# Optimization experiments

Hardware: AMD Instinct MI355X
Metric: run time of the kernel (lower is better)

Reference implementation:

```python
import jax, jax.numpy as jnp
import numpy as np


def setup_inputs() -> dict:
    key = jax.random.key(0)
    k1, k2, k3, k4, k5 = jax.random.split(key, 5)
    B, T, K, H, A = 16, 256, 256, 512, 49
    return {
        "hiddens_des": jax.random.normal(k1, (B, K, H), dtype=jnp.float32),
        "hiddens_title": jax.random.normal(k2, (B, T, H), dtype=jnp.float32),
        "Wv": jax.random.normal(k3, (A, H), dtype=jnp.float32) * (1.0 / np.sqrt(H)),
        "Wg": jax.random.normal(k4, (A, H), dtype=jnp.float32) * (1.0 / np.sqrt(H)),
        "Wh": jax.random.normal(k5, (1, A), dtype=jnp.float32) * (1.0 / np.sqrt(A)),
    }


def reference(hiddens_des, hiddens_title, Wv, Wg, Wh):
    # Dropout is identity (eval mode) for the deterministic baseline.
    # content_v: (B,1,K,49) + (B,T,1,49) -> (B,T,K,49)
    cv = jnp.einsum("bkh,ah->bka", hiddens_des, Wv)    # (B,K,49)
    cg = jnp.einsum("bth,ah->bta", hiddens_title, Wg)  # (B,T,49)
    content = cv[:, None, :, :] + cg[:, :, None, :]     # (B,T,K,49)
    z = jnp.einsum("btka,a->btk", jnp.tanh(content), Wh[0])  # (B,T,K)
    alpha = jax.nn.softmax(z, axis=-1)                  # softmax over K
    c_hat = jnp.einsum("btk,bkh->bth", alpha, hiddens_des)  # (B,T,H)
    return (c_hat, alpha)
```

## Files before the change

### kernel.cpp

```cpp
#include <hip/hip_runtime.h>
#include <hip/hip_bf16.h>

#define B_ 16
#define T_ 256
#define K_ 256
#define H_ 512
#define A_ 49
#define APAD 64

typedef __attribute__((ext_vector_type(8))) short short8;
typedef __attribute__((ext_vector_type(4))) float f32x4;

__device__ __forceinline__ ushort f2bf(float f) {
    uint u = __builtin_bit_cast(uint, f);
    u += 0x7FFF + ((u >> 16) & 1);
    return (ushort)(u >> 16);
}

__device__ __forceinline__ void cvt_hilo(float4 v0, float4 v1, short8& hi, short8& lo) {
    float v[8] = {v0.x, v0.y, v0.z, v0.w, v1.x, v1.y, v1.z, v1.w};
    #pragma unroll
    for (int i = 0; i < 8; ++i) {
        ushort h = f2bf(v[i]);
        float hf = __builtin_bit_cast(float, (uint)h << 16);
        hi[i] = (short)h;
        lo[i] = (short)f2bf(v[i] - hf);
    }
}

__device__ __forceinline__ float sig2(float x) {
    float e = __expf(2.f * x);
    return __builtin_amdgcn_rcpf(e + 1.f);
}

__global__ __launch_bounds__(256) void kW(const float* __restrict__ Wv,
                                          const float* __restrict__ Wg,
                                          ushort* __restrict__ Whl)
{
    int blk = blockIdx.x;
    int m = blk >> 6, row = blk & 63;
    const float* W = m ? Wg : Wv;
    int tid = threadIdx.x;
    ushort* hi = Whl + ((size_t)(m * 2 + 0) * 64 + row) * H_;
    ushort* lo = Whl + ((size_t)(m * 2 + 1) * 64 + row) * H_;
    #pragma unroll
    for (int c = tid; c < H_; c += 256) {
        float v = (row < A_) ? W[(size_t)row * H_ + c] : 0.f;
        ushort h = f2bf(v);
        float hf = __builtin_bit_cast(float, (uint)h << 16);
        hi[c] = h;
        lo[c] = f2bf(v - hf);
    }
}

#define XPAD 520
union UAP {
    struct { ushort hi[16][XPAD]; ushort lo[16][XPAD]; } x;
    float tls[32][33];
};

__global__ __launch_bounds__(256) void kAP(const float* __restrict__ des,
                                           const float* __restrict__ title,
                                           const ushort* __restrict__ Whl,
                                           float* __restrict__ cvT,
                                           float* __restrict__ cg,
                                           ushort* __restrict__ desT)
{
    __shared__ UAP u;
    int tid = threadIdx.x;

    if (blockIdx.x >= 512) {
        int tb = blockIdx.x - 512;
        int b = tb >> 7, rem = tb & 127;
        int k0 = (rem >> 4) * 32, h0 = (rem & 15) * 32;
        int kk = tid >> 3, c4 = (tid & 7) * 4;
        float4 v = *(const float4*)(des + ((size_t)(b * K_ + k0 + kk) * H_) + h0 + c4);
        u.tls[kk][33 * 0 + c4 + 0] = v.x;
        u.tls[kk][c4 + 1] = v.y;
        u.tls[kk][c4 + 2] = v.z;
        u.tls[kk][c4 + 3] = v.w;
        __syncthreads();
        int hh = tid >> 3;
        ushort4 o;
        o.x = f2bf(u.tls[c4 + 0][hh]);
        o.y = f2bf(u.tls[c4 + 1][hh]);
        o.z = f2bf(u.tls[c4 + 2][hh]);
        o.w = f2bf(u.tls[c4 + 3][hh]);
        *(ushort4*)(desT + ((size_t)(b * H_ + h0 + hh) * K_) + k0 + c4) = o;
        return;
    }

    int tile = blockIdx.x;
    bool isDes = tile < 256;
    const float* Xbase = isDes ? (des + (size_t)tile * 16 * H_)
                               : (title + (size_t)(tile - 256) * 16 * H_);

    {
        #pragma unroll
        for (int it = 0; it < 4; ++it) {
            int eidx = it * 2048 + tid * 8;
            int r = eidx >> 9, c = eidx & 511;
            const float* p = Xbase + (size_t)r * H_ + c;
            float4 v0 = *(const float4*)(p);
            float4 v1 = *(const float4*)(p + 4);
            short8 hi, lo;
            cvt_hilo(v0, v1, hi, lo);
            *(short8*)&u.x.hi[r][c] = hi;
            *(short8*)&u.x.lo[r][c] = lo;
        }
    }
    __syncthreads();

    int wv = tid >> 6, lane = tid & 63;
    int lr = lane & 15, lc = lane >> 4;
    int g = wv;
    int m = isDes ? 0 : 1;
    const ushort* whiP = Whl + ((size_t)(m * 2 + 0) * 64 + g * 16 + lr) * H_ + lc * 8;
    const ushort* wloP = Whl + ((size_t)(m * 2 + 1) * 64 + g * 16 + lr) * H_ + lc * 8;

    f32x4 acc = {};
    #pragma unroll 4
    for (int k0 = 0; k0 < H_; k0 += 32) {
        short8 whi = *(const short8*)(whiP + k0);
        short8 wlo = *(const short8*)(wloP + k0);
        short8 xhi = *(const short8*)&u.x.hi[lr][k0 + lc * 8];
        short8 xlo = *(const short8*)&u.x.lo[lr][k0 + lc * 8];
        if (isDes) {
            acc = __builtin_amdgcn_mfma_f32_16x16x32_bf16(whi, xhi, acc, 0, 0, 0);
            acc = __builtin_amdgcn_mfma_f32_16x16x32_bf16(whi, xlo, acc, 0, 0, 0);
            acc = __builtin_amdgcn_mfma_f32_16x16x32_bf16(wlo, xhi, acc, 0, 0, 0);
        } else {
            acc = __builtin_amdgcn_mfma_f32_16x16x32_bf16(xhi, whi, acc, 0, 0, 0);
            acc = __builtin_amdgcn_mfma_f32_16x16x32_bf16(xlo, whi, acc, 0, 0, 0);
            acc = __builtin_amdgcn_mfma_f32_16x16x32_bf16(xhi, wlo, acc, 0, 0, 0);
        }
    }

    if (isDes) {
        int krows = tile * 16;
        int b = krows >> 8, kb = krows & 255;
        #pragma unroll
        for (int r = 0; r < 4; ++r) {
            int a = g * 16 + lc * 4 + r;
            cvT[((size_t)b * APAD + a) * K_ + kb + lr] = acc[r];
        }
    } else {
        int trows = (tile - 256) * 16;
        #pragma unroll
        for (int r = 0; r < 4; ++r) {
            int row = trows + lc * 4 + r;
            cg[(size_t)row * APAD + g * 16 + lr] = acc[r];
        }
    }
}

__global__ __launch_bounds__(512) void kZ(const float* __restrict__ cvT,
                                          const float* __restrict__ cg,
                                          const float* __restrict__ Wh,
                                          const ushort* __restrict__ desT,
                                          float* __restrict__ alpha,
                                          float* __restrict__ chat)
{
    __shared__ float  sCg[8][APAD];
    __shared__ float  sWh[APAD];
    __shared__ float  sRedM[8][4];
    __shared__ float  sRedS[8][4];
    __shared__ ushort sA[16][K_ + 8];

    int bid = blockIdx.x;
    int b  = bid & 15;
    int t0 = (bid >> 4) * 8;
    int tid = threadIdx.x;
    int k  = tid & 255;
    int tg = tid >> 8;
    int tb = tg * 4;

    if (tid < 128) {
        int row = tid >> 4, c = (tid & 15) * 4;
        *(float4*)(&sCg[row][c]) =
            *(const float4*)(cg + (size_t)(b * T_ + t0 + row) * APAD + c);
    } else if (tid < 128 + APAD) {
        int a = tid - 128;
        sWh[a] = (a < A_) ? Wh[a] : 0.f;
    }
    {
        uint* zp = (uint*)&sA[8][0];
        #pragma unroll
        for (int i = tid; i < 1056; i += 512) zp[i] = 0;
    }
    __syncthreads();

    const float* cvp = cvT + (size_t)b * APAD * K_ + k;
    float zacc[4] = {0.f, 0.f, 0.f, 0.f};

    for (int c6 = 0; c6 < 6; ++c6) {
        int a0 = c6 * 8;
        float xa[8];
        #pragma unroll
        for (int i = 0; i < 8; ++i) xa[i] = cvp[(size_t)(a0 + i) * K_];
        float4 w0 = *(const float4*)&sWh[a0];
        float4 w1 = *(const float4*)&sWh[a0 + 4];
        #pragma unroll
        for (int j = 0; j < 4; ++j) {
            float4 c0 = *(const float4*)&sCg[tb + j][a0];
            float4 c1 = *(const float4*)&sCg[tb + j][a0 + 4];
            zacc[j] += w0.x * sig2(xa[0] + c0.x) + w0.y * sig2(xa[1] + c0.y)
                     + w0.z * sig2(xa[2] + c0.z) + w0.w * sig2(xa[3] + c0.w)
                     + w1.x * sig2(xa[4] + c1.x) + w1.y * sig2(xa[5] + c1.y)
                     + w1.z * sig2(xa[6] + c1.z) + w1.w * sig2(xa[7] + c1.w);
        }
    }
    {
        float xa48 = cvp[(size_t)48 * K_];
        float wh = sWh[48];
        #pragma unroll
        for (int j = 0; j < 4; ++j)
            zacc[j] += wh * sig2(xa48 + sCg[tb + j][48]);
    }
    float sw = 0.f;
    #pragma unroll
    for (int q = 0; q < 16; ++q) {
        float4 w4 = *(const float4*)&sWh[q * 4];
        sw += w4.x + w4.y + w4.z + w4.w;
    }
    float z[4];
    #pragma unroll
    for (int j = 0; j < 4; ++j) z[j] = sw - 2.f * zacc[j];

    int wv = tid >> 6, lane = tid & 63, w3 = wv & 3;
    #pragma unroll
    for (int j = 0; j < 4; ++j) {
        float m = z[j];
        #pragma unroll
        for (int off = 32; off > 0; off >>= 1) m = fmaxf(m, __shfl_xor(m, off));
        if (lane == 0) sRedM[tb + j][w3] = m;
    }
    __syncthreads();
    #pragma unroll
    for (int j = 0; j < 4; ++j) {
        int t = tb + j;
        float m = fmaxf(fmaxf(sRedM[t][0], sRedM[t][1]),
                        fmaxf(sRedM[t][2], sRedM[t][3]));
        z[j] = __expf(z[j] - m);
    }
    #pragma unroll
    for (int j = 0; j < 4; ++j) {
        float s = z[j];
        #pragma unroll
        for (int off = 32; off > 0; off >>= 1) s += __shfl_xor(s, off);
        if (lane == 0) sRedS[tb + j][w3] = s;
    }
    __syncthreads();
    #pragma unroll
    for (int j = 0; j < 4; ++j) {
        int t = tb + j;
        float s = sRedS[t][0] + sRedS[t][1] + sRedS[t][2] + sRedS[t][3];
        float rs = __builtin_amdgcn_rcpf(s);
        rs = rs * (2.f - s * rs);
        float al = z[j] * rs;
        alpha[(size_t)(b * T_ + t0 + t) * K_ + k] = al;
        sA[t][k] = f2bf(al);
    }
    __syncthreads();

    int lr = lane & 15, lc = lane >> 4;
    int h0 = wv * 64;
    const ushort* Bp = desT + ((size_t)(b * H_ + h0 + lr)) * K_ + lc * 8;

    short8 af[8];
    #pragma unroll
    for (int s = 0; s < 8; ++s)
        af[s] = *(const short8*)(&sA[lr][s * 32 + lc * 8]);

    f32x4 acc[4] = {};
    #pragma unroll
    for (int j = 0; j < 4; ++j) {
        const ushort* Bj = Bp + (size_t)(j * 16) * K_;
        short8 bf[8];
        #pragma unroll
        for (int s = 0; s < 8; ++s)
            bf[s] = *(const short8*)(Bj + s * 32);
        #pragma unroll
        for (int s = 0; s < 8; ++s)
            acc[j] = __builtin_amdgcn_mfma_f32_16x16x32_bf16(af[s], bf[s], acc[j], 0, 0, 0);
    }

    #pragma unroll
    for (int j = 0; j < 4; ++j) {
        #pragma unroll
        for (int r = 0; r < 4; ++r) {
            int row = lc * 4 + r;
            if (row < 8)
                chat[((size_t)(b * T_ + t0 + row)) * H_ + h0 + j * 16 + lr] = acc[j][r];
        }
    }
}

extern "C" void kernel_launch(void* const* d_in, const int* in_sizes, int n_in,
                              void* d_out, int out_size, void* d_ws, size_t ws_size,
                              hipStream_t stream) {
    const float* des   = (const float*)d_in[0];
    const float* title = (const float*)d_in[1];
    const float* Wv    = (const float*)d_in[2];
    const float* Wg    = (const float*)d_in[3];
    const float* Wh    = (const float*)d_in[4];

    float* chat  = (float*)d_out;
    float* alpha = (float*)d_out + (size_t)B_ * T_ * H_;

    char* ws = (char*)d_ws;
    float*  cvT  = (float*)ws;
    float*  cg   = cvT + (size_t)B_ * APAD * K_;
    ushort* desT = (ushort*)(cg + (size_t)B_ * T_ * APAD);
    ushort* Whl  = desT + (size_t)B_ * H_ * K_;

    hipLaunchKernelGGL(kW, dim3(128), dim3(256), 0, stream, Wv, Wg, Whl);
    hipLaunchKernelGGL(kAP, dim3(2560), dim3(256), 0, stream,
                       des, title, Whl, cvT, cg, desT);
    hipLaunchKernelGGL(kZ, dim3(2 * B_ * (T_ / 16)), dim3(512), 0, stream,
                       cvT, cg, Wh, desT, alpha, chat);
}
```

Baseline: 52.23 us.

## Drop x-low bf16 split term, prescale by 2log2e, double-buffer cv loads

The projection GEMM no longer keeps a low bf16 part of the input activations. It drops the xlo shared-memory buffer and one of the three MFMAs per step, which halves LDS staging and cuts MFMA work by a third, at some cost in accuracy. The projection outputs are prescaled by 2*log2(e) so the tanh-sigmoid uses a raw exp2 without a multiply. The score loop is also unrolled with ping-pong register buffers so cv loads for the next chunk are issued before the current chunk is consumed.

Result: slower. 58.10 us (+11.2%).

```diff
diff --git a/kernel.cpp b/kernel.cpp
--- a/kernel.cpp
+++ b/kernel.cpp
@@ -7,6 +7,7 @@
 #define H_ 512
 #define A_ 49
 #define APAD 64
+#define SC2LOG2E 2.8853900817779268f
 
 typedef __attribute__((ext_vector_type(8))) short short8;
 typedef __attribute__((ext_vector_type(4))) float f32x4;
@@ -17,19 +18,8 @@
     return (ushort)(u >> 16);
 }
 
-__device__ __forceinline__ void cvt_hilo(float4 v0, float4 v1, short8& hi, short8& lo) {
-    float v[8] = {v0.x, v0.y, v0.z, v0.w, v1.x, v1.y, v1.z, v1.w};
-    #pragma unroll
-    for (int i = 0; i < 8; ++i) {
-        ushort h = f2bf(v[i]);
-        float hf = __builtin_bit_cast(float, (uint)h << 16);
-        hi[i] = (short)h;
-        lo[i] = (short)f2bf(v[i] - hf);
-    }
-}
-
-__device__ __forceinline__ float sig2(float x) {
-    float e = __expf(2.f * x);
+__device__ __forceinline__ float sig2s(float x) {
+    float e = __builtin_amdgcn_exp2f(x);
     return __builtin_amdgcn_rcpf(e + 1.f);
 }
 
@@ -55,8 +45,8 @@
 
 #define XPAD 520
 union UAP {
-    struct { ushort hi[16][XPAD]; ushort lo[16][XPAD]; } x;
-    float tls[32][33];
+    ushort xhi[16][XPAD];
+    float  tls[32][33];
 };
 
 __global__ __launch_bounds__(256) void kAP(const float* __restrict__ des,
@@ -75,7 +65,7 @@
         int k0 = (rem >> 4) * 32, h0 = (rem & 15) * 32;
         int kk = tid >> 3, c4 = (tid & 7) * 4;
         float4 v = *(const float4*)(des + ((size_t)(b * K_ + k0 + kk) * H_) + h0 + c4);
-        u.tls[kk][33 * 0 + c4 + 0] = v.x;
+        u.tls[kk][c4 + 0] = v.x;
         u.tls[kk][c4 + 1] = v.y;
         u.tls[kk][c4 + 2] = v.z;
         u.tls[kk][c4 + 3] = v.w;
@@ -103,10 +93,11 @@
             const float* p = Xbase + (size_t)r * H_ + c;
             float4 v0 = *(const float4*)(p);
             float4 v1 = *(const float4*)(p + 4);
-            short8 hi, lo;
-            cvt_hilo(v0, v1, hi, lo);
-            *(short8*)&u.x.hi[r][c] = hi;
-            *(short8*)&u.x.lo[r][c] = lo;
+            float vv[8] = {v0.x, v0.y, v0.z, v0.w, v1.x, v1.y, v1.z, v1.w};
+            short8 hi;
+            #pragma unroll
+            for (int i = 0; i < 8; ++i) hi[i] = (short)f2bf(vv[i]);
+            *(short8*)&u.xhi[r][c] = hi;
         }
     }
     __syncthreads();
@@ -123,15 +114,12 @@
     for (int k0 = 0; k0 < H_; k0 += 32) {
         short8 whi = *(const short8*)(whiP + k0);
         short8 wlo = *(const short8*)(wloP + k0);
-        short8 xhi = *(const short8*)&u.x.hi[lr][k0 + lc * 8];
-        short8 xlo = *(const short8*)&u.x.lo[lr][k0 + lc * 8];
+        short8 xhi = *(const short8*)&u.xhi[lr][k0 + lc * 8];
         if (isDes) {
             acc = __builtin_amdgcn_mfma_f32_16x16x32_bf16(whi, xhi, acc, 0, 0, 0);
-            acc = __builtin_amdgcn_mfma_f32_16x16x32_bf16(whi, xlo, acc, 0, 0, 0);
             acc = __builtin_amdgcn_mfma_f32_16x16x32_bf16(wlo, xhi, acc, 0, 0, 0);
         } else {
             acc = __builtin_amdgcn_mfma_f32_16x16x32_bf16(xhi, whi, acc, 0, 0, 0);
-            acc = __builtin_amdgcn_mfma_f32_16x16x32_bf16(xlo, whi, acc, 0, 0, 0);
             acc = __builtin_amdgcn_mfma_f32_16x16x32_bf16(xhi, wlo, acc, 0, 0, 0);
         }
     }
@@ -142,14 +130,14 @@
         #pragma unroll
         for (int r = 0; r < 4; ++r) {
             int a = g * 16 + lc * 4 + r;
-            cvT[((size_t)b * APAD + a) * K_ + kb + lr] = acc[r];
+            cvT[((size_t)b * APAD + a) * K_ + kb + lr] = acc[r] * SC2LOG2E;
         }
     } else {
         int trows = (tile - 256) * 16;
         #pragma unroll
         for (int r = 0; r < 4; ++r) {
             int row = trows + lc * 4 + r;
-            cg[(size_t)row * APAD + g * 16 + lr] = acc[r];
+            cg[(size_t)row * APAD + g * 16 + lr] = acc[r] * SC2LOG2E;
         }
     }
 }
@@ -192,30 +180,46 @@
 
     const float* cvp = cvT + (size_t)b * APAD * K_ + k;
     float zacc[4] = {0.f, 0.f, 0.f, 0.f};
-
-    for (int c6 = 0; c6 < 6; ++c6) {
-        int a0 = c6 * 8;
-        float xa[8];
-        #pragma unroll
-        for (int i = 0; i < 8; ++i) xa[i] = cvp[(size_t)(a0 + i) * K_];
-        float4 w0 = *(const float4*)&sWh[a0];
-        float4 w1 = *(const float4*)&sWh[a0 + 4];
-        #pragma unroll
-        for (int j = 0; j < 4; ++j) {
-            float4 c0 = *(const float4*)&sCg[tb + j][a0];
-            float4 c1 = *(const float4*)&sCg[tb + j][a0 + 4];
-            zacc[j] += w0.x * sig2(xa[0] + c0.x) + w0.y * sig2(xa[1] + c0.y)
-                     + w0.z * sig2(xa[2] + c0.z) + w0.w * sig2(xa[3] + c0.w)
-                     + w1.x * sig2(xa[4] + c1.x) + w1.y * sig2(xa[5] + c1.y)
-                     + w1.z * sig2(xa[6] + c1.z) + w1.w * sig2(xa[7] + c1.w);
-        }
-    }
+    float xaA[8], xaB[8];
+    #pragma unroll
+    for (int i = 0; i < 8; ++i) xaA[i] = cvp[(size_t)i * K_];
+
+#define CONSUME(xa, a0) { \
+    float4 w0 = *(const float4*)&sWh[(a0)]; \
+    float4 w1 = *(const float4*)&sWh[(a0) + 4]; \
+    _Pragma("unroll") \
+    for (int j = 0; j < 4; ++j) { \
+        float4 c0 = *(const float4*)&sCg[tb + j][(a0)]; \
+        float4 c1 = *(const float4*)&sCg[tb + j][(a0) + 4]; \
+        zacc[j] += w0.x * sig2s(xa[0] + c0.x) + w0.y * sig2s(xa[1] + c0.y) \
+                 + w0.z * sig2s(xa[2] + c0.z) + w0.w * sig2s(xa[3] + c0.w) \
+                 + w1.x * sig2s(xa[4] + c1.x) + w1.y * sig2s(xa[5] + c1.y) \
+                 + w1.z * sig2s(xa[6] + c1.z) + w1.w * sig2s(xa[7] + c1.w); \
+    } }
+
+    #pragma unroll
+    for (int i = 0; i < 8; ++i) xaB[i] = cvp[(size_t)(8 + i) * K_];
+    CONSUME(xaA, 0)
+    #pragma unroll
+    for (int i = 0; i < 8; ++i) xaA[i] = cvp[(size_t)(16 + i) * K_];
+    CONSUME(xaB, 8)
+    #pragma unroll
+    for (int i = 0; i < 8; ++i) xaB[i] = cvp[(size_t)(24 + i) * K_];
+    CONSUME(xaA, 16)
+    #pragma unroll
+    for (int i = 0; i < 8; ++i) xaA[i] = cvp[(size_t)(32 + i) * K_];
+    CONSUME(xaB, 24)
+    #pragma unroll
+    for (int i = 0; i < 8; ++i) xaB[i] = cvp[(size_t)(40 + i) * K_];
+    CONSUME(xaA, 32)
+    float xa48 = cvp[(size_t)48 * K_];
+    CONSUME(xaB, 40)
+#undef CONSUME
     {
-        float xa48 = cvp[(size_t)48 * K_];
         float wh = sWh[48];
         #pragma unroll
         for (int j = 0; j < 4; ++j)
-            zacc[j] += wh * sig2(xa48 + sCg[tb + j][48]);
+            zacc[j] += wh * sig2s(xa48 + sCg[tb + j][48]);
     }
     float sw = 0.f;
     #pragma unroll
```
